# Kernel optimization log

Hardware: AMD Instinct MI355X
Metric: run time of the kernel (lower is better)

Reference implementation:

```python
import jax, jax.numpy as jnp
import numpy as np

N = 20000
MOL = 16
MH = 64      # message_hidden
UH = 64      # update_hidden
HEADS = 2
CUTOFF = 0.02257
E_FIX = 720000
REL_IN = 3 + 2 + MOL          # 21
SELF_F = 2 + MOL + 1 + 1      # 20
EDGE_A = MH + SELF_F          # 84
OUT_D = 2 + 1 + MOL + 1       # 20


def _build_edges(x_np, cutoff):
    """All ordered pairs (i,j), i!=j, with dist<=cutoff (matches symmetrized triu in torch)."""
    src_l, dst_l = [], []
    chunk = 1000
    Nn = x_np.shape[0]
    c2 = cutoff * cutoff
    for i0 in range(0, Nn, chunk):
        xi = x_np[i0:i0 + chunk]
        d2 = ((xi[:, None, :] - x_np[None, :, :]) ** 2).sum(-1)
        ii, jj = np.nonzero(d2 <= c2)
        ii = ii + i0
        keep = ii != jj
        dst_l.append(ii[keep])
        src_l.append(jj[keep])
    return (np.concatenate(src_l).astype(np.int32),
            np.concatenate(dst_l).astype(np.int32))


def setup_inputs() -> dict:
    key = jax.random.key(0)
    ks = jax.random.split(key, 30)
    x = jax.random.uniform(ks[0], (N, 2), dtype=jnp.float32)
    angle = jax.random.normal(ks[1], (N, 1), dtype=jnp.float32)
    molecules = jax.random.normal(ks[2], (N, MOL), dtype=jnp.float32)
    generation = jnp.zeros((N, 1), dtype=jnp.float32)

    src_np, dst_np = _build_edges(np.asarray(x), CUTOFF)
    E = min(src_np.shape[0], E_FIX)
    src = np.zeros(E_FIX, np.int32)
    dst = np.zeros(E_FIX, np.int32)
    mask = np.zeros(E_FIX, np.float32)
    src[:E] = src_np[:E]
    dst[:E] = dst_np[:E]
    mask[:E] = 1.0

    def p(k, shape):
        return jax.random.normal(k, shape, dtype=jnp.float32) * 0.05

    inp = dict(
        x=x, angle=angle, molecules=molecules, generation=generation,
        src=jnp.asarray(src), dst=jnp.asarray(dst), edge_mask=jnp.asarray(mask),
        # message_mlp
        mw1=p(ks[3], (REL_IN, MH)), mb1=p(ks[4], (MH,)),
        mw2=p(ks[5], (MH, MH)), mb2=p(ks[6], (MH,)),
        mw3=p(ks[7], (MH, MH)), mb3=p(ks[8], (MH,)),
        # TransformerConv (heads=2, out=UH, concat=False, edge_dim=EDGE_A)
        wq=p(ks[9], (SELF_F, HEADS * UH)), bq=p(ks[10], (HEADS * UH,)),
        wk=p(ks[11], (SELF_F, HEADS * UH)), bk=p(ks[12], (HEADS * UH,)),
        wv=p(ks[13], (SELF_F, HEADS * UH)), bv=p(ks[14], (HEADS * UH,)),
        we=p(ks[15], (EDGE_A, HEADS * UH)),  # lin_edge has no bias in PyG
        wskip=p(ks[16], (SELF_F, UH)), bskip=p(ks[17], (UH,)),
        # node_head
        hw1=p(ks[18], (UH, UH)), hb1=p(ks[19], (UH,)),
        hw2=p(ks[20], (UH, UH)), hb2=p(ks[21], (UH,)),
        hw3=p(ks[22], (UH, OUT_D)), hb3=p(ks[23], (OUT_D,)),
    )
    return inp


def reference(x, angle, molecules, generation, src, dst, edge_mask,
              mw1, mb1, mw2, mb2, mw3, mb3,
              wq, bq, wk, bk, wv, bv, we, wskip, bskip,
              hw1, hb1, hw2, hb2, hw3, hb3):
    Nn = x.shape[0]
    H, C = HEADS, UH
    m = edge_mask  # [E], 1 for real edges, 0 for padding

    # relative edge features (j = src = neighbor, i = dst = center)
    dxdy = x[src] - x[dst]                                          # [E,2]
    r = jnp.sqrt(jnp.clip((dxdy ** 2).sum(-1, keepdims=True), 1e-12))
    d_ang = angle[src] - angle[dst]                                 # [E,1]
    d_mol = molecules[src] - molecules[dst]                         # [E,MOL]
    rel_in = jnp.concatenate([dxdy, r, jnp.sin(d_ang), jnp.cos(d_ang), d_mol], -1)

    h = jax.nn.relu(rel_in @ mw1 + mb1)
    h = jax.nn.relu(h @ mw2 + mb2)
    msg = jax.nn.relu(h @ mw3 + mb3)                                # [E,MH]

    degree = jax.ops.segment_sum(m, dst, num_segments=Nn)[:, None]  # [N,1]
    self_feat = jnp.concatenate(
        [jnp.sin(angle), jnp.cos(angle), molecules, generation, degree], -1)  # [N,20]
    edge_attr = jnp.concatenate([msg, self_feat[dst]], -1)          # [E,84]

    # TransformerConv: q_i, (k_j + e), (v_j + e); per-dst segment softmax; mean heads; + skip
    q = (self_feat @ wq + bq).reshape(Nn, H, C)
    k = (self_feat @ wk + bk).reshape(Nn, H, C)
    v = (self_feat @ wv + bv).reshape(Nn, H, C)
    e = (edge_attr @ we).reshape(-1, H, C)
    key_e = k[src] + e
    val_e = v[src] + e
    alpha = (q[dst] * key_e).sum(-1) / jnp.sqrt(jnp.float32(C))     # [E,H]
    alpha = jnp.where(m[:, None] > 0, alpha, -1e9)
    amax = jax.ops.segment_max(alpha, dst, num_segments=Nn)         # [N,H]
    ex = jnp.exp(alpha - amax[dst]) * m[:, None]
    denom = jax.ops.segment_sum(ex, dst, num_segments=Nn)           # [N,H]
    w = ex / (denom[dst] + 1e-16)                                   # [E,H]
    out = jax.ops.segment_sum(val_e * w[:, :, None], dst, num_segments=Nn)  # [N,H,C]
    out = out.mean(axis=1) + (self_feat @ wskip + bskip)            # [N,UH]

    u = jax.nn.relu(out @ hw1 + hb1)
    u = jax.nn.relu(u @ hw2 + hb2)
    upd = u @ hw3 + hb3                                             # [N,20]

    return (upd[:, 0:2], upd[:, 2:3], upd[:, 3:3 + MOL], upd[:, 3 + MOL:4 + MOL])
```

## Files before the change

### kernel.cpp

```cpp
#include <hip/hip_runtime.h>
#include <hip/hip_bf16.h>
#include <math.h>

#define NN 20000
#define EF 720000

typedef float  f4 __attribute__((ext_vector_type(4)));
typedef unsigned int u4 __attribute__((ext_vector_type(4)));

__device__ __forceinline__ void MFMA(f4& c, u4 a, u4 b) {
    asm("v_mfma_f32_16x16x32_bf16 %0, %1, %2, %0" : "+v"(c) : "v"(a), "v"(b));
}

__device__ __forceinline__ unsigned pk(float a, float b) {
    __hip_bfloat162 t = __halves2bfloat162(__float2bfloat16(a), __float2bfloat16(b));
    unsigned u; __builtin_memcpy(&u, &t, 4); return u;
}
__device__ __forceinline__ float bf2f(unsigned short u) {
    return __builtin_bit_cast(float, (unsigned)u << 16);
}
__device__ __forceinline__ f4 bf2f4(ushort4 u) {
    f4 r; r.x = bf2f(u.x); r.y = bf2f(u.y); r.z = bf2f(u.z); r.w = bf2f(u.w); return r;
}
__device__ __forceinline__ float dot4(f4 a, f4 b) {
    return a.x * b.x + a.y * b.y + a.z * b.z + a.w * b.w;
}
__device__ __forceinline__ void fma4(f4& acc, float w, f4 v) {
    acc.x += w * v.x; acc.y += w * v.y; acc.z += w * v.z; acc.w += w * v.w;
}

__global__ __launch_bounds__(256) void k_prep(
    const float* __restrict__ mw1, const float* __restrict__ mb1,
    const float* __restrict__ mw2, const float* __restrict__ mw3,
    const float* __restrict__ hw1, const float* __restrict__ hw2, const float* __restrict__ hw3,
    const float* __restrict__ we, const float* __restrict__ wk, const float* __restrict__ bk,
    const float* __restrict__ wv, const float* __restrict__ bv,
    const float* __restrict__ wq, const float* __restrict__ bq,
    __hip_bfloat16* __restrict__ W1b, __hip_bfloat16* __restrict__ W2b, __hip_bfloat16* __restrict__ W3b,
    __hip_bfloat16* __restrict__ H1b, __hip_bfloat16* __restrict__ H2b, __hip_bfloat16* __restrict__ H3b,
    __hip_bfloat16* __restrict__ WcA, float* __restrict__ Mwe, float* __restrict__ Mk)
{
    int t = blockIdx.x * 256 + threadIdx.x;
    if (t < 2048) {
        int ch = t >> 5, k = t & 31;
        float v = (k < 21) ? mw1[k * 64 + ch] : (k == 21 ? mb1[ch] : 0.f);
        W1b[t] = __float2bfloat16(v); return;
    }
    t -= 2048;
    if (t < 4096) { int ch = t >> 6, k = t & 63; W2b[t] = __float2bfloat16(mw2[k * 64 + ch]); return; }
    t -= 4096;
    if (t < 4096) { int ch = t >> 6, k = t & 63; W3b[t] = __float2bfloat16(mw3[k * 64 + ch]); return; }
    t -= 4096;
    if (t < 4096) { int ch = t >> 6, k = t & 63; H1b[t] = __float2bfloat16(hw1[k * 64 + ch]); return; }
    t -= 4096;
    if (t < 4096) { int ch = t >> 6, k = t & 63; H2b[t] = __float2bfloat16(hw2[k * 64 + ch]); return; }
    t -= 4096;
    if (t < 2048) {
        int ch = t >> 6, k = t & 63;
        float v = (ch < 20) ? hw3[k * 20 + ch] : 0.f;
        H3b[t] = __float2bfloat16(v); return;
    }
    t -= 2048;
    if (t < 16384) {
        int h = t >> 13, rem = t & 8191;
        int ch = rem >> 7, k = rem & 127;
        int col = h * 64 + ch;
        float v;
        if (k < 64)        v = we[k * 128 + col];
        else if (k < 84)   v = wv[(k - 64) * 128 + col];
        else if (k == 84)  v = bv[col];
        else if (k < 96)   v = 0.f;
        else if (k < 116)  v = we[(64 + (k - 96)) * 128 + col];
        else               v = 0.f;
        WcA[t] = __float2bfloat16(v); return;
    }
    t -= 16384;
    if (t < 3528) {
        int j = t / 168, o = t % 168;
        int h = (o >= 84) ? 1 : 0, a = o - 84 * h;
        float acc = 0.f;
        for (int c = 0; c < 64; c++) {
            int hc = h * 64 + c;
            float wqv = (j < 20) ? wq[j * 128 + hc] : bq[hc];
            acc += wqv * we[a * 128 + hc];
        }
        Mwe[t] = acc; return;
    }
    t -= 3528;
    if (t < 1344) {
        int j = t / 64, rem = t % 64;
        int h = rem >> 5, a = rem & 31;
        float acc = 0.f;
        if (a <= 20) {
            for (int c = 0; c < 64; c++) {
                int hc = h * 64 + c;
                float wqv = (j < 20) ? wq[j * 128 + hc] : bq[hc];
                float wkv = (a < 20) ? wk[a * 128 + hc] : bk[hc];
                acc += wqv * wkv;
            }
        }
        Mk[t] = acc; return;
    }
}

__global__ __launch_bounds__(256) void k_csr(
    const int* __restrict__ dst, const float* __restrict__ mask, int* __restrict__ row_off)
{
    int n = blockIdx.x * 256 + threadIdx.x;
    if (n > NN) return;
    int lo = 0, hi = EF;
    while (lo < hi) { int mid = (lo + hi) >> 1; if (mask[mid] > 0.5f) lo = mid + 1; else hi = mid; }
    int Ea = lo;
    lo = 0; hi = Ea;
    while (lo < hi) { int mid = (lo + hi) >> 1; if (dst[mid] < n) lo = mid + 1; else hi = mid; }
    row_off[n] = lo;
}

__global__ __launch_bounds__(256) void k_node(
    const float* __restrict__ angle, const float* __restrict__ mol, const float* __restrict__ gen,
    const int* __restrict__ row_off,
    const float* __restrict__ wskip, const float* __restrict__ bskip,
    const float* __restrict__ Mwe, const float* __restrict__ Mk,
    float* __restrict__ selff, __hip_bfloat16* __restrict__ selffb,
    float* __restrict__ skipf, float* __restrict__ qwe, float* __restrict__ qkp)
{
    int wid = threadIdx.x >> 6, lane = threadIdx.x & 63;
    int n = blockIdx.x * 4 + wid;

    float an = angle[n];
    float sv, cv; sincosf(an, &sv, &cv);
    float degf = (float)(row_off[n + 1] - row_off[n]);
    float sfa[21];
    sfa[0] = sv; sfa[1] = cv;
#pragma unroll
    for (int j = 0; j < 16; j++) sfa[2 + j] = mol[n * 16 + j];
    sfa[18] = gen[n];
    sfa[19] = degf;
    sfa[20] = 1.f;

    float sval = (lane == 0) ? sv : (lane == 1) ? cv :
                 (lane < 18) ? mol[n * 16 + (lane - 2)] :
                 (lane == 18) ? gen[n] : degf;
    if (lane < 20) selff[n * 20 + lane] = sval;
    if (lane < 32) {
        float v = (lane < 20) ? sval : (lane == 20 ? 1.f : 0.f);
        selffb[n * 32 + lane] = __float2bfloat16(v);
    }

    float sk = bskip[lane];
#pragma unroll
    for (int j = 0; j < 20; j++) sk += sfa[j] * wskip[j * 64 + lane];
    skipf[n * 64 + lane] = sk;

#pragma unroll
    for (int r = 0; r < 3; r++) {
        int o = r * 64 + lane;
        if (o < 168) {
            float acc = 0.f;
#pragma unroll
            for (int j = 0; j < 21; j++) acc += sfa[j] * Mwe[j * 168 + o];
            qwe[n * 168 + o] = acc;
        }
    }

    {
        float acc = 0.f;
#pragma unroll
        for (int j = 0; j < 21; j++) acc += sfa[j] * Mk[j * 64 + lane];
        qkp[n * 64 + lane] = acc;
    }
}

__device__ __forceinline__ void write_tiles(char* lds, int l, f4 (&acc)[4][4], const float* bias)
{
#pragma unroll
    for (int m = 0; m < 4; m++) {
        f4 bv;
        if (bias) bv = *(const f4*)(bias + m * 16 + ((l >> 4) << 2));
        else      { bv.x = 0.f; bv.y = 0.f; bv.z = 0.f; bv.w = 0.f; }
#pragma unroll
        for (int n = 0; n < 4; n++) {
            f4 v = acc[m][n];
            float v0 = fmaxf(v.x + bv.x, 0.f);
            float v1 = fmaxf(v.y + bv.y, 0.f);
            float v2 = fmaxf(v.z + bv.z, 0.f);
            float v3 = fmaxf(v.w + bv.w, 0.f);
            int e   = n * 16 + (l & 15);
            int ch0 = m * 16 + ((l >> 4) << 2);
            int byte = e * 128 + ((((ch0 >> 3) ^ (e & 7))) << 4) + (ch0 & 7) * 2;
            uint2 w; w.x = pk(v0, v1); w.y = pk(v2, v3);
            *(uint2*)(lds + byte) = w;
        }
    }
}

__global__ __launch_bounds__(256) void k_edge_mfma(
    const float* __restrict__ x, const float* __restrict__ angle, const float* __restrict__ mol,
    const int* __restrict__ src, const int* __restrict__ dst,
    const float* __restrict__ mask,
    const __hip_bfloat16* __restrict__ W1b, const __hip_bfloat16* __restrict__ W2b,
    const __hip_bfloat16* __restrict__ W3b,
    const float* __restrict__ mb2, const float* __restrict__ mb3,
    __hip_bfloat16* __restrict__ msg)
{
    __shared__ char lds_all[4][64 * 128];
    int wv = threadIdx.x >> 6, l = threadIdx.x & 63;
    char* lds = lds_all[wv];
    int e0 = (blockIdx.x * 4 + wv) * 64;
    if (e0 + 64 > EF) e0 = EF - 64;

    if (mask[e0] < 0.5f) return;

    int s = src[e0 + l], d = dst[e0 + l];
    float2 xs = ((const float2*)x)[s], xd = ((const float2*)x)[d];
    float dx = xs.x - xd.x, dy = xs.y - xd.y;
    float r = sqrtf(fmaxf(dx * dx + dy * dy, 1e-12f));
    float da = angle[s] - angle[d];
    float sv, cv; sincosf(da, &sv, &cv);
    const float4* m4 = (const float4*)mol;
    float4 sa = m4[s * 4 + 0], sb = m4[s * 4 + 1], sc = m4[s * 4 + 2], sd = m4[s * 4 + 3];
    float4 ta = m4[d * 4 + 0], tb = m4[d * 4 + 1], tc = m4[d * 4 + 2], td = m4[d * 4 + 3];
    float f[22];
    f[0] = dx; f[1] = dy; f[2] = r; f[3] = sv; f[4] = cv;
    f[5]  = sa.x - ta.x; f[6]  = sa.y - ta.y; f[7]  = sa.z - ta.z; f[8]  = sa.w - ta.w;
    f[9]  = sb.x - tb.x; f[10] = sb.y - tb.y; f[11] = sb.z - tb.z; f[12] = sb.w - tb.w;
    f[13] = sc.x - tc.x; f[14] = sc.y - tc.y; f[15] = sc.z - tc.z; f[16] = sc.w - tc.w;
    f[17] = sd.x - td.x; f[18] = sd.y - td.y; f[19] = sd.z - td.z; f[20] = sd.w - td.w;
    f[21] = 1.f;
    unsigned p[16];
#pragma unroll
    for (int j = 0; j < 11; j++) p[j] = pk(f[2 * j], f[2 * j + 1]);
#pragma unroll
    for (int j = 11; j < 16; j++) p[j] = 0u;
#pragma unroll
    for (int g = 0; g < 4; g++) {
        int byte = l * 64 + ((g ^ (l & 3)) << 4);
        u4 w; w.x = p[4 * g]; w.y = p[4 * g + 1]; w.z = p[4 * g + 2]; w.w = p[4 * g + 3];
        *(u4*)(lds + byte) = w;
    }

    u4 B1[4];
#pragma unroll
    for (int n = 0; n < 4; n++) {
        int e = n * 16 + (l & 15);
        int byte = e * 64 + ((((l >> 4) & 3) ^ (e & 3)) << 4);
        B1[n] = *(const u4*)(lds + byte);
    }

    f4 acc[4][4];
#pragma unroll
    for (int m = 0; m < 4; m++)
#pragma unroll
        for (int n = 0; n < 4; n++) { acc[m][n].x = 0.f; acc[m][n].y = 0.f; acc[m][n].z = 0.f; acc[m][n].w = 0.f; }

    const unsigned short* W1u = (const unsigned short*)W1b;
    const unsigned short* W2u = (const unsigned short*)W2b;
    const unsigned short* W3u = (const unsigned short*)W3b;
#pragma unroll
    for (int m = 0; m < 4; m++) {
        u4 w = *(const u4*)(W1u + (m * 16 + (l & 15)) * 32 + (l >> 4) * 8);
#pragma unroll
        for (int n = 0; n < 4; n++) MFMA(acc[m][n], w, B1[n]);
    }
    write_tiles(lds, l, acc, nullptr);

    u4 B2[4][2];
#pragma unroll
    for (int n = 0; n < 4; n++)
#pragma unroll
        for (int ks = 0; ks < 2; ks++) {
            int e = n * 16 + (l & 15);
            int g = ks * 4 + (l >> 4);
            B2[n][ks] = *(const u4*)(lds + e * 128 + ((g ^ (e & 7)) << 4));
        }
#pragma unroll
    for (int m = 0; m < 4; m++)
#pragma unroll
        for (int n = 0; n < 4; n++) { acc[m][n].x = 0.f; acc[m][n].y = 0.f; acc[m][n].z = 0.f; acc[m][n].w = 0.f; }
#pragma unroll
    for (int m = 0; m < 4; m++)
#pragma unroll
        for (int ks = 0; ks < 2; ks++) {
            u4 w = *(const u4*)(W2u + (m * 16 + (l & 15)) * 64 + ks * 32 + (l >> 4) * 8);
#pragma unroll
            for (int n = 0; n < 4; n++) MFMA(acc[m][n], w, B2[n][ks]);
        }
    write_tiles(lds, l, acc, mb2);

#pragma unroll
    for (int n = 0; n < 4; n++)
#pragma unroll
        for (int ks = 0; ks < 2; ks++) {
            int e = n * 16 + (l & 15);
            int g = ks * 4 + (l >> 4);
            B2[n][ks] = *(const u4*)(lds + e * 128 + ((g ^ (e & 7)) << 4));
        }
#pragma unroll
    for (int m = 0; m < 4; m++)
#pragma unroll
        for (int n = 0; n < 4; n++) { acc[m][n].x = 0.f; acc[m][n].y = 0.f; acc[m][n].z = 0.f; acc[m][n].w = 0.f; }
#pragma unroll
    for (int m = 0; m < 4; m++)
#pragma unroll
        for (int ks = 0; ks < 2; ks++) {
            u4 w = *(const u4*)(W3u + (m * 16 + (l & 15)) * 64 + ks * 32 + (l >> 4) * 8);
#pragma unroll
            for (int n = 0; n < 4; n++) MFMA(acc[m][n], w, B2[n][ks]);
        }
    write_tiles(lds, l, acc, mb3);

#pragma unroll
    for (int it = 0; it < 8; it++) {
        int e = it * 8 + (l >> 3);
        int g = l & 7;
        u4 vv = *(const u4*)(lds + e * 128 + ((g ^ (e & 7)) << 4));
        *(u4*)((unsigned short*)msg + (size_t)(e0 + e) * 64 + g * 8) = vv;
    }
}

__global__ __launch_bounds__(256) void k_attn(
    const int* __restrict__ row_off, const int* __restrict__ src,
    const __hip_bfloat16* __restrict__ msg,
    const __hip_bfloat16* __restrict__ selffb, const float* __restrict__ qkp,
    const float* __restrict__ qwe, const float* __restrict__ selff,
    __hip_bfloat16* __restrict__ agg, float* __restrict__ invp)
{
    int tid = threadIdx.x, wid = tid >> 6, lane = tid & 63;
    int g = lane >> 4, c16 = lane & 15;
    int n = blockIdx.x * 4 + wid;

    f4 qm0 = *(const f4*)(qwe + n * 168 + 4 * c16);
    f4 qm1 = *(const f4*)(qwe + n * 168 + 84 + 4 * c16);
    float2 qk0 = *(const float2*)(qkp + n * 64 + 2 * c16);
    float2 qk1 = *(const float2*)(qkp + n * 64 + 32 + 2 * c16);

    float a00 = 0.f, a01 = 0.f;
#pragma unroll
    for (int j = 0; j < 20; j++) {
        float sfj = selff[n * 20 + j];
        a00 += sfj * qwe[n * 168 + 64 + j];
        a01 += sfj * qwe[n * 168 + 84 + 64 + j];
    }

    const unsigned short* msgu = (const unsigned short*)msg;
    const unsigned short* sfu  = (const unsigned short*)selffb;
    int r0 = row_off[n], r1 = row_off[n + 1];
    int nit = (r1 - r0 + 3) >> 2;

    f4 Wm0 = {0,0,0,0}, Wm1 = {0,0,0,0};
    float Ws00 = 0.f, Ws01 = 0.f, Ws10 = 0.f, Ws11 = 0.f;
    float S0 = 0.f, S1 = 0.f;

#pragma unroll 2
    for (int it = 0; it < nit; it++) {
        int e = r0 + it * 4 + g;
        bool ok = (e < r1);
        int ec = ok ? e : r0;
        int s = src[ec];
        ushort2 su = *(const ushort2*)(sfu + (size_t)s * 32 + 2 * c16);
        float sf0 = bf2f(su.x), sf1 = bf2f(su.y);
        f4 mc = bf2f4(*(const ushort4*)(msgu + (size_t)ec * 64 + 4 * c16));

        float t0 = dot4(qm0, mc) + sf0 * qk0.x + sf1 * qk0.y;
        float t1 = dot4(qm1, mc) + sf0 * qk1.x + sf1 * qk1.y;
#pragma unroll
        for (int mk = 1; mk < 16; mk <<= 1) {
            t0 += __shfl_xor(t0, mk, 64);
            t1 += __shfl_xor(t1, mk, 64);
        }
        float w0 = ok ? __expf((t0 + a00) * 0.125f) : 0.f;
        float w1 = ok ? __expf((t1 + a01) * 0.125f) : 0.f;
        S0 += w0; S1 += w1;
        fma4(Wm0, w0, mc); fma4(Wm1, w1, mc);
        Ws00 += w0 * sf0; Ws01 += w0 * sf1;
        Ws10 += w1 * sf0; Ws11 += w1 * sf1;
    }

#pragma unroll
    for (int mk = 16; mk <= 32; mk <<= 1) {
        Wm0.x += __shfl_xor(Wm0.x, mk, 64); Wm0.y += __shfl_xor(Wm0.y, mk, 64);
        Wm0.z += __shfl_xor(Wm0.z, mk, 64); Wm0.w += __shfl_xor(Wm0.w, mk, 64);
        Wm1.x += __shfl_xor(Wm1.x, mk, 64); Wm1.y += __shfl_xor(Wm1.y, mk, 64);
        Wm1.z += __shfl_xor(Wm1.z, mk, 64); Wm1.w += __shfl_xor(Wm1.w, mk, 64);
        Ws00 += __shfl_xor(Ws00, mk, 64); Ws01 += __shfl_xor(Ws01, mk, 64);
        Ws10 += __shfl_xor(Ws10, mk, 64); Ws11 += __shfl_xor(Ws11, mk, 64);
        S0 += __shfl_xor(S0, mk, 64); S1 += __shfl_xor(S1, mk, 64);
    }

    unsigned short* arow = (unsigned short*)agg + (size_t)n * 256;
    if (g == 0) {
        uint2 w; w.x = pk(Wm0.x, Wm0.y); w.y = pk(Wm0.z, Wm0.w);
        *(uint2*)(arow + 4 * c16) = w;
        int j0 = 2 * c16, j1 = 2 * c16 + 1;
        float v0 = (j0 < 20) ? S0 * selff[n * 20 + j0] : 0.f;
        float v1 = (j1 < 20) ? S0 * selff[n * 20 + j1] : 0.f;
        *(unsigned*)(arow + 96 + 2 * c16) = pk(v0, v1);
    } else if (g == 1) {
        uint2 w; w.x = pk(Wm1.x, Wm1.y); w.y = pk(Wm1.z, Wm1.w);
        *(uint2*)(arow + 128 + 4 * c16) = w;
        int j0 = 2 * c16, j1 = 2 * c16 + 1;
        float v0 = (j0 < 20) ? S1 * selff[n * 20 + j0] : 0.f;
        float v1 = (j1 < 20) ? S1 * selff[n * 20 + j1] : 0.f;
        *(unsigned*)(arow + 128 + 96 + 2 * c16) = pk(v0, v1);
    } else if (g == 2) {
        *(unsigned*)(arow + 64 + 2 * c16) = pk(Ws00, Ws01);
        if (c16 == 0) invp[2 * n] = 1.f / (S0 + 1e-16f);
    } else {
        *(unsigned*)(arow + 128 + 64 + 2 * c16) = pk(Ws10, Ws11);
        if (c16 == 0) invp[2 * n + 1] = 1.f / (S1 + 1e-16f);
    }
}

__global__ __launch_bounds__(64) void k_final2(
    const __hip_bfloat16* __restrict__ agg, const float* __restrict__ invp,
    const float* __restrict__ skipf, const __hip_bfloat16* __restrict__ WcA,
    const __hip_bfloat16* __restrict__ H1b, const __hip_bfloat16* __restrict__ H2b,
    const __hip_bfloat16* __restrict__ H3b,
    const float* __restrict__ hb1, const float* __restrict__ hb2, const float* __restrict__ hb3,
    float* __restrict__ out)
{
    __shared__ char lds[64 * 128];
    int l = threadIdx.x;
    int n0 = blockIdx.x * 64;

    const unsigned short* aggU = (const unsigned short*)agg;
    const unsigned short* WcU = (const unsigned short*)WcA;
    const unsigned short* H1u = (const unsigned short*)H1b;
    const unsigned short* H2u = (const unsigned short*)H2b;
    const unsigned short* H3u = (const unsigned short*)H3b;

    int nodes[4];
    float inv0[4], inv1[4];
#pragma unroll
    for (int n4 = 0; n4 < 4; n4++) {
        int node = n0 + n4 * 16 + (l & 15); if (node >= NN) node = NN - 1;
        nodes[n4] = node;
        float2 iv = *(const float2*)(invp + 2 * node);
        inv0[n4] = iv.x; inv1[n4] = iv.y;
    }

    f4 osum[4][4];
#pragma unroll
    for (int m = 0; m < 4; m++)
#pragma unroll
        for (int n4 = 0; n4 < 4; n4++) { osum[m][n4].x = 0.f; osum[m][n4].y = 0.f; osum[m][n4].z = 0.f; osum[m][n4].w = 0.f; }

#pragma unroll
    for (int h = 0; h < 2; h++) {
        f4 acc[4][4];
#pragma unroll
        for (int m = 0; m < 4; m++)
#pragma unroll
            for (int n4 = 0; n4 < 4; n4++) { acc[m][n4].x = 0.f; acc[m][n4].y = 0.f; acc[m][n4].z = 0.f; acc[m][n4].w = 0.f; }
#pragma unroll
        for (int ks = 0; ks < 4; ks++) {
            u4 A[4];
#pragma unroll
            for (int m = 0; m < 4; m++)
                A[m] = *(const u4*)(WcU + h * 8192 + (m * 16 + (l & 15)) * 128 + ks * 32 + (l >> 4) * 8);
#pragma unroll
            for (int n4 = 0; n4 < 4; n4++) {
                u4 B = *(const u4*)(aggU + (size_t)nodes[n4] * 256 + h * 128 + ks * 32 + (l >> 4) * 8);
#pragma unroll
                for (int m = 0; m < 4; m++) MFMA(acc[m][n4], A[m], B);
            }
        }
        const float* iv = h ? inv1 : inv0;
#pragma unroll
        for (int m = 0; m < 4; m++)
#pragma unroll
            for (int n4 = 0; n4 < 4; n4++) fma4(osum[m][n4], 0.5f * iv[n4], acc[m][n4]);
    }

#pragma unroll
    for (int m = 0; m < 4; m++) {
#pragma unroll
        for (int n4 = 0; n4 < 4; n4++) {
            int ch0 = m * 16 + ((l >> 4) << 2);
            float4 sk = *(const float4*)(skipf + (size_t)nodes[n4] * 64 + ch0);
            f4 v = osum[m][n4];
            float v0 = v.x + sk.x, v1 = v.y + sk.y, v2 = v.z + sk.z, v3 = v.w + sk.w;
            int e = n4 * 16 + (l & 15);
            int byte = e * 128 + ((((ch0 >> 3) ^ (e & 7))) << 4) + (ch0 & 7) * 2;
            uint2 w; w.x = pk(v0, v1); w.y = pk(v2, v3);
            *(uint2*)(lds + byte) = w;
        }
    }
    __syncthreads();

    u4 B[4][2];
    f4 acc[4][4];

#pragma unroll
    for (int n = 0; n < 4; n++)
#pragma unroll
        for (int ks = 0; ks < 2; ks++) {
            int e = n * 16 + (l & 15);
            int g = ks * 4 + (l >> 4);
            B[n][ks] = *(const u4*)(lds + e * 128 + ((g ^ (e & 7)) << 4));
        }
    __syncthreads();
#pragma unroll
    for (int m = 0; m < 4; m++)
#pragma unroll
        for (int n = 0; n < 4; n++) { acc[m][n].x = 0.f; acc[m][n].y = 0.f; acc[m][n].z = 0.f; acc[m][n].w = 0.f; }
#pragma unroll
    for (int m = 0; m < 4; m++)
#pragma unroll
        for (int ks = 0; ks < 2; ks++) {
            u4 w = *(const u4*)(H1u + (m * 16 + (l & 15)) * 64 + ks * 32 + (l >> 4) * 8);
#pragma unroll
            for (int n = 0; n < 4; n++) MFMA(acc[m][n], w, B[n][ks]);
        }
    write_tiles(lds, l, acc, hb1);
    __syncthreads();

#pragma unroll
    for (int n = 0; n < 4; n++)
#pragma unroll
        for (int ks = 0; ks < 2; ks++) {
            int e = n * 16 + (l & 15);
            int g = ks * 4 + (l >> 4);
            B[n][ks] = *(const u4*)(lds + e * 128 + ((g ^ (e & 7)) << 4));
        }
    __syncthreads();
#pragma unroll
    for (int m = 0; m < 4; m++)
#pragma unroll
        for (int n = 0; n < 4; n++) { acc[m][n].x = 0.f; acc[m][n].y = 0.f; acc[m][n].z = 0.f; acc[m][n].w = 0.f; }
#pragma unroll
    for (int m = 0; m < 4; m++)
#pragma unroll
        for (int ks = 0; ks < 2; ks++) {
            u4 w = *(const u4*)(H2u + (m * 16 + (l & 15)) * 64 + ks * 32 + (l >> 4) * 8);
#pragma unroll
            for (int n = 0; n < 4; n++) MFMA(acc[m][n], w, B[n][ks]);
        }
    write_tiles(lds, l, acc, hb2);
    __syncthreads();

#pragma unroll
    for (int n = 0; n < 4; n++)
#pragma unroll
        for (int ks = 0; ks < 2; ks++) {
            int e = n * 16 + (l & 15);
            int g = ks * 4 + (l >> 4);
            B[n][ks] = *(const u4*)(lds + e * 128 + ((g ^ (e & 7)) << 4));
        }

    f4 acc3[2][4];
#pragma unroll
    for (int m = 0; m < 2; m++)
#pragma unroll
        for (int n = 0; n < 4; n++) { acc3[m][n].x = 0.f; acc3[m][n].y = 0.f; acc3[m][n].z = 0.f; acc3[m][n].w = 0.f; }
#pragma unroll
    for (int m = 0; m < 2; m++)
#pragma unroll
        for (int ks = 0; ks < 2; ks++) {
            u4 w = *(const u4*)(H3u + (m * 16 + (l & 15)) * 64 + ks * 32 + (l >> 4) * 8);
#pragma unroll
            for (int n = 0; n < 4; n++) MFMA(acc3[m][n], w, B[n][ks]);
        }

#pragma unroll
    for (int m = 0; m < 2; m++) {
#pragma unroll
        for (int j = 0; j < 4; j++) {
            int ch = m * 16 + (l >> 4) * 4 + j;
            if (ch < 20) {
                float b = hb3[ch];
#pragma unroll
                for (int nt = 0; nt < 4; nt++) {
                    int node = n0 + nt * 16 + (l & 15);
                    if (node < NN) {
                        float v = acc3[m][nt][j] + b;
                        if (ch < 2)       out[node * 2 + ch] = v;
                        else if (ch == 2) out[2 * NN + node] = v;
                        else if (ch < 19) out[3 * NN + node * 16 + (ch - 3)] = v;
                        else              out[19 * NN + node] = v;
                    }
                }
            }
        }
    }
}

extern "C" void kernel_launch(void* const* d_in, const int* in_sizes, int n_in,
                              void* d_out, int out_size, void* d_ws, size_t ws_size,
                              hipStream_t stream)
{
    const float* x      = (const float*)d_in[0];
    const float* angle  = (const float*)d_in[1];
    const float* mol    = (const float*)d_in[2];
    const float* gen    = (const float*)d_in[3];
    const int*   src    = (const int*)d_in[4];
    const int*   dst    = (const int*)d_in[5];
    const float* mask   = (const float*)d_in[6];
    const float* mw1    = (const float*)d_in[7];
    const float* mb1    = (const float*)d_in[8];
    const float* mw2    = (const float*)d_in[9];
    const float* mb2    = (const float*)d_in[10];
    const float* mw3    = (const float*)d_in[11];
    const float* mb3    = (const float*)d_in[12];
    const float* wq     = (const float*)d_in[13];
    const float* bq     = (const float*)d_in[14];
    const float* wk     = (const float*)d_in[15];
    const float* bk     = (const float*)d_in[16];
    const float* wv     = (const float*)d_in[17];
    const float* bv     = (const float*)d_in[18];
    const float* we     = (const float*)d_in[19];
    const float* wskip  = (const float*)d_in[20];
    const float* bskip  = (const float*)d_in[21];
    const float* hw1    = (const float*)d_in[22];
    const float* hb1    = (const float*)d_in[23];
    const float* hw2    = (const float*)d_in[24];
    const float* hb2    = (const float*)d_in[25];
    const float* hw3    = (const float*)d_in[26];
    const float* hb3    = (const float*)d_in[27];
    float* out = (float*)d_out;

    char* p = (char*)d_ws;
    auto alloc = [&](size_t bytes) -> void* {
        void* r = (void*)p;
        p += (bytes + 255) & ~(size_t)255;
        return r;
    };
    int*   row_off = (int*)alloc((NN + 1) * 4);
    float* selff   = (float*)alloc((size_t)NN * 20 * 4);
    __hip_bfloat16* selffb = (__hip_bfloat16*)alloc((size_t)NN * 32 * 2);
    float* qkp     = (float*)alloc((size_t)NN * 64 * 4);
    float* skipf   = (float*)alloc((size_t)NN * 64 * 4);
    float* qwe     = (float*)alloc((size_t)NN * 168 * 4);
    __hip_bfloat16* agg = (__hip_bfloat16*)alloc((size_t)NN * 256 * 2);
    float* invp    = (float*)alloc((size_t)NN * 2 * 4);
    __hip_bfloat16* W1b = (__hip_bfloat16*)alloc(2048 * 2);
    __hip_bfloat16* W2b = (__hip_bfloat16*)alloc(4096 * 2);
    __hip_bfloat16* W3b = (__hip_bfloat16*)alloc(4096 * 2);
    __hip_bfloat16* H1b = (__hip_bfloat16*)alloc(4096 * 2);
    __hip_bfloat16* H2b = (__hip_bfloat16*)alloc(4096 * 2);
    __hip_bfloat16* H3b = (__hip_bfloat16*)alloc(2048 * 2);
    __hip_bfloat16* WcA = (__hip_bfloat16*)alloc(16384 * 2);
    float* Mwe     = (float*)alloc(3528 * 4);
    float* Mk      = (float*)alloc(1344 * 4);
    __hip_bfloat16* msg = (__hip_bfloat16*)alloc((size_t)EF * 64 * 2);

    k_prep<<<164, 256, 0, stream>>>(mw1, mb1, mw2, mw3, hw1, hw2, hw3, we, wk, bk, wv, bv,
                                    wq, bq, W1b, W2b, W3b, H1b, H2b, H3b, WcA, Mwe, Mk);
    k_csr<<<(NN + 256) / 256, 256, 0, stream>>>(dst, mask, row_off);
    k_node<<<NN / 4, 256, 0, stream>>>(angle, mol, gen, row_off,
                                       wskip, bskip, Mwe, Mk,
                                       selff, selffb, skipf, qwe, qkp);
    k_edge_mfma<<<(EF / 64 + 3) / 4, 256, 0, stream>>>(x, angle, mol, src, dst, mask,
                                                       W1b, W2b, W3b, mb2, mb3, msg);
    k_attn<<<NN / 4, 256, 0, stream>>>(row_off, src, msg, selffb, qkp,
                                       qwe, selff, agg, invp);
    k_final2<<<(NN + 63) / 64, 64, 0, stream>>>(agg, invp, skipf, WcA,
                                                H1b, H2b, H3b, hb1, hb2, hb3, out);
}
```

Measured before the change: 146.0 us.

## Process eight edges per wavefront iteration in attention with 8-lane groups

The attention kernel now assigns 8 lanes per edge, so each lane holds 8 message channels, instead of 16 lanes with 4 channels each. A wavefront therefore handles 8 edges per loop iteration, and each lane issues one 16-byte message load. The qwe row stride is padded from 168 to 192 so the per-head query vectors stay 16-byte aligned, which means the prep and node kernels change to match. The intent is fewer loop iterations and shorter reduction chains per edge, in exchange for more registers per lane and more cross-lane shuffles in the final reduction.

```diff
diff --git a/kernel.cpp b/kernel.cpp
--- a/kernel.cpp
+++ b/kernel.cpp
@@ -19,14 +19,9 @@
 __device__ __forceinline__ float bf2f(unsigned short u) {
     return __builtin_bit_cast(float, (unsigned)u << 16);
 }
-__device__ __forceinline__ f4 bf2f4(ushort4 u) {
-    f4 r; r.x = bf2f(u.x); r.y = bf2f(u.y); r.z = bf2f(u.z); r.w = bf2f(u.w); return r;
-}
-__device__ __forceinline__ float dot4(f4 a, f4 b) {
-    return a.x * b.x + a.y * b.y + a.z * b.z + a.w * b.w;
-}
-__device__ __forceinline__ void fma4(f4& acc, float w, f4 v) {
-    acc.x += w * v.x; acc.y += w * v.y; acc.z += w * v.z; acc.w += w * v.w;
+__device__ __forceinline__ unsigned short f2bfu(float f) {
+    __hip_bfloat16 b = __float2bfloat16(f);
+    unsigned short u; __builtin_memcpy(&u, &b, 2); return u;
 }
 
 __global__ __launch_bounds__(256) void k_prep(
@@ -75,18 +70,20 @@
         WcA[t] = __float2bfloat16(v); return;
     }
     t -= 16384;
-    if (t < 3528) {
-        int j = t / 168, o = t % 168;
-        int h = (o >= 84) ? 1 : 0, a = o - 84 * h;
+    if (t < 4032) {
+        int j = t / 192, o = t % 192;
+        int h = (o >= 96) ? 1 : 0, a = o - 96 * h;
         float acc = 0.f;
-        for (int c = 0; c < 64; c++) {
-            int hc = h * 64 + c;
-            float wqv = (j < 20) ? wq[j * 128 + hc] : bq[hc];
-            acc += wqv * we[a * 128 + hc];
+        if (a < 84) {
+            for (int c = 0; c < 64; c++) {
+                int hc = h * 64 + c;
+                float wqv = (j < 20) ? wq[j * 128 + hc] : bq[hc];
+                acc += wqv * we[a * 128 + hc];
+            }
         }
         Mwe[t] = acc; return;
     }
-    t -= 3528;
+    t -= 4032;
     if (t < 1344) {
         int j = t / 64, rem = t % 64;
         int h = rem >> 5, a = rem & 31;
@@ -155,12 +152,10 @@
 #pragma unroll
     for (int r = 0; r < 3; r++) {
         int o = r * 64 + lane;
-        if (o < 168) {
-            float acc = 0.f;
-#pragma unroll
-            for (int j = 0; j < 21; j++) acc += sfa[j] * Mwe[j * 168 + o];
-            qwe[n * 168 + o] = acc;
-        }
+        float acc = 0.f;
+#pragma unroll
+        for (int j = 0; j < 21; j++) acc += sfa[j] * Mwe[j * 192 + o];
+        qwe[n * 192 + o] = acc;
     }
 
     {
@@ -326,88 +321,118 @@
     __hip_bfloat16* __restrict__ agg, float* __restrict__ invp)
 {
     int tid = threadIdx.x, wid = tid >> 6, lane = tid & 63;
-    int g = lane >> 4, c16 = lane & 15;
+    int g = lane >> 3, c8 = lane & 7;
     int n = blockIdx.x * 4 + wid;
 
-    f4 qm0 = *(const f4*)(qwe + n * 168 + 4 * c16);
-    f4 qm1 = *(const f4*)(qwe + n * 168 + 84 + 4 * c16);
-    float2 qk0 = *(const float2*)(qkp + n * 64 + 2 * c16);
-    float2 qk1 = *(const float2*)(qkp + n * 64 + 32 + 2 * c16);
+    const float* qrow = qwe + (size_t)n * 192;
+    f4 qmA0 = *(const f4*)(qrow + 8 * c8);
+    f4 qmA1 = *(const f4*)(qrow + 8 * c8 + 4);
+    f4 qmB0 = *(const f4*)(qrow + 96 + 8 * c8);
+    f4 qmB1 = *(const f4*)(qrow + 96 + 8 * c8 + 4);
+    float qk0a = qkp[n * 64 + c8],      qk0b = qkp[n * 64 + c8 + 8],      qk0c = qkp[n * 64 + c8 + 16];
+    float qk1a = qkp[n * 64 + 32 + c8], qk1b = qkp[n * 64 + 32 + c8 + 8], qk1c = qkp[n * 64 + 32 + c8 + 16];
 
     float a00 = 0.f, a01 = 0.f;
 #pragma unroll
     for (int j = 0; j < 20; j++) {
         float sfj = selff[n * 20 + j];
-        a00 += sfj * qwe[n * 168 + 64 + j];
-        a01 += sfj * qwe[n * 168 + 84 + 64 + j];
+        a00 += sfj * qrow[64 + j];
+        a01 += sfj * qrow[96 + 64 + j];
     }
 
     const unsigned short* msgu = (const unsigned short*)msg;
     const unsigned short* sfu  = (const unsigned short*)selffb;
     int r0 = row_off[n], r1 = row_off[n + 1];
-    int nit = (r1 - r0 + 3) >> 2;
-
-    f4 Wm0 = {0,0,0,0}, Wm1 = {0,0,0,0};
-    float Ws00 = 0.f, Ws01 = 0.f, Ws10 = 0.f, Ws11 = 0.f;
+    int nit = (r1 - r0 + 7) >> 3;
+
+    f4 WmA0 = {0,0,0,0}, WmA1 = {0,0,0,0}, WmB0 = {0,0,0,0}, WmB1 = {0,0,0,0};
+    float Ws0a = 0.f, Ws0b = 0.f, Ws0c = 0.f, Ws1a = 0.f, Ws1b = 0.f, Ws1c = 0.f;
     float S0 = 0.f, S1 = 0.f;
 
 #pragma unroll 2
     for (int it = 0; it < nit; it++) {
-        int e = r0 + it * 4 + g;
+        int e = r0 + it * 8 + g;
         bool ok = (e < r1);
         int ec = ok ? e : r0;
         int s = src[ec];
-        ushort2 su = *(const ushort2*)(sfu + (size_t)s * 32 + 2 * c16);
-        float sf0 = bf2f(su.x), sf1 = bf2f(su.y);
-        f4 mc = bf2f4(*(const ushort4*)(msgu + (size_t)ec * 64 + 4 * c16));
-
-        float t0 = dot4(qm0, mc) + sf0 * qk0.x + sf1 * qk0.y;
-        float t1 = dot4(qm1, mc) + sf0 * qk1.x + sf1 * qk1.y;
-#pragma unroll
-        for (int mk = 1; mk < 16; mk <<= 1) {
+        float sfA = bf2f(sfu[(size_t)s * 32 + c8]);
+        float sfB = bf2f(sfu[(size_t)s * 32 + c8 + 8]);
+        float sfC = bf2f(sfu[(size_t)s * 32 + c8 + 16]);
+        u4 mr = *(const u4*)(msgu + (size_t)ec * 64 + 8 * c8);
+        float c0 = __builtin_bit_cast(float, mr.x << 16);
+        float c1 = __builtin_bit_cast(float, mr.x & 0xffff0000u);
+        float c2 = __builtin_bit_cast(float, mr.y << 16);
+        float c3 = __builtin_bit_cast(float, mr.y & 0xffff0000u);
+        float c4 = __builtin_bit_cast(float, mr.z << 16);
+        float c5 = __builtin_bit_cast(float, mr.z & 0xffff0000u);
+        float c6 = __builtin_bit_cast(float, mr.w << 16);
+        float c7 = __builtin_bit_cast(float, mr.w & 0xffff0000u);
+
+        float t0 = qmA0.x * c0 + qmA0.y * c1 + qmA0.z * c2 + qmA0.w * c3
+                 + qmA1.x * c4 + qmA1.y * c5 + qmA1.z * c6 + qmA1.w * c7
+                 + sfA * qk0a + sfB * qk0b + sfC * qk0c;
+        float t1 = qmB0.x * c0 + qmB0.y * c1 + qmB0.z * c2 + qmB0.w * c3
+                 + qmB1.x * c4 + qmB1.y * c5 + qmB1.z * c6 + qmB1.w * c7
+                 + sfA * qk1a + sfB * qk1b + sfC * qk1c;
+#pragma unroll
+        for (int mk = 1; mk < 8; mk <<= 1) {
             t0 += __shfl_xor(t0, mk, 64);
             t1 += __shfl_xor(t1, mk, 64);
         }
         float w0 = ok ? __expf((t0 + a00) * 0.125f) : 0.f;
         float w1 = ok ? __expf((t1 + a01) * 0.125f) : 0.f;
         S0 += w0; S1 += w1;
-        fma4(Wm0, w0, mc); fma4(Wm1, w1, mc);
-        Ws00 += w0 * sf0; Ws01 += w0 * sf1;
-        Ws10 += w1 * sf0; Ws11 += w1 * sf1;
-    }
-
-#pragma unroll
-    for (int mk = 16; mk <= 32; mk <<= 1) {
-        Wm0.x += __shfl_xor(Wm0.x, mk, 64); Wm0.y += __shfl_xor(Wm0.y, mk, 64);
-        Wm0.z += __shfl_xor(Wm0.z, mk, 64); Wm0.w += __shfl_xor(Wm0.w, mk, 64);
-        Wm1.x += __shfl_xor(Wm1.x, mk, 64); Wm1.y += __shfl_xor(Wm1.y, mk, 64);
-        Wm1.z += __shfl_xor(Wm1.z, mk, 64); Wm1.w += __shfl_xor(Wm1.w, mk, 64);
-        Ws00 += __shfl_xor(Ws00, mk, 64); Ws01 += __shfl_xor(Ws01, mk, 64);
-        Ws10 += __shfl_xor(Ws10, mk, 64); Ws11 += __shfl_xor(Ws11, mk, 64);
+        WmA0.x += w0 * c0; WmA0.y += w0 * c1; WmA0.z += w0 * c2; WmA0.w += w0 * c3;
+        WmA1.x += w0 * c4; WmA1.y += w0 * c5; WmA1.z += w0 * c6; WmA1.w += w0 * c7;
+        WmB0.x += w1 * c0; WmB0.y += w1 * c1; WmB0.z += w1 * c2; WmB0.w += w1 * c3;
+        WmB1.x += w1 * c4; WmB1.y += w1 * c5; WmB1.z += w1 * c6; WmB1.w += w1 * c7;
+        Ws0a += w0 * sfA; Ws0b += w0 * sfB; Ws0c += w0 * sfC;
+        Ws1a += w1 * sfA; Ws1b += w1 * sfB; Ws1c += w1 * sfC;
+    }
+
+#pragma unroll
+    for (int mk = 8; mk <= 32; mk <<= 1) {
+        WmA0.x += __shfl_xor(WmA0.x, mk, 64); WmA0.y += __shfl_xor(WmA0.y, mk, 64);
+        WmA0.z += __shfl_xor(WmA0.z, mk, 64); WmA0.w += __shfl_xor(WmA0.w, mk, 64);
+        WmA1.x += __shfl_xor(WmA1.x, mk, 64); WmA1.y += __shfl_xor(WmA1.y, mk, 64);
+        WmA1.z += __shfl_xor(WmA1.z, mk, 64); WmA1.w += __shfl_xor(WmA1.w, mk, 64);
+        WmB0.x += __shfl_xor(WmB0.x, mk, 64); WmB0.y += __shfl_xor(WmB0.y, mk, 64);
+        WmB0.z += __shfl_xor(WmB0.z, mk, 64); WmB0.w += __shfl_xor(WmB0.w, mk, 64);
+        WmB1.x += __shfl_xor(WmB1.x, mk, 64); WmB1.y += __shfl_xor(WmB1.y, mk, 64);
+        WmB1.z += __shfl_xor(WmB1.z, mk, 64); WmB1.w += __shfl_xor(WmB1.w, mk, 64);
+        Ws0a += __shfl_xor(Ws0a, mk, 64); Ws0b += __shfl_xor(Ws0b, mk, 64); Ws0c += __shfl_xor(Ws0c, mk, 64);
+        Ws1a += __shfl_xor(Ws1a, mk, 64); Ws1b += __shfl_xor(Ws1b, mk, 64); Ws1c += __shfl_xor(Ws1c, mk, 64);
         S0 += __shfl_xor(S0, mk, 64); S1 += __shfl_xor(S1, mk, 64);
     }
 
     unsigned short* arow = (unsigned short*)agg + (size_t)n * 256;
     if (g == 0) {
-        uint2 w; w.x = pk(Wm0.x, Wm0.y); w.y = pk(Wm0.z, Wm0.w);
-        *(uint2*)(arow + 4 * c16) = w;
-        int j0 = 2 * c16, j1 = 2 * c16 + 1;
-        float v0 = (j0 < 20) ? S0 * selff[n * 20 + j0] : 0.f;
-        float v1 = (j1 < 20) ? S0 * selff[n * 20 + j1] : 0.f;
-        *(unsigned*)(arow + 96 + 2 * c16) = pk(v0, v1);
+        u4 w; w.x = pk(WmA0.x, WmA0.y); w.y = pk(WmA0.z, WmA0.w);
+        w.z = pk(WmA1.x, WmA1.y); w.w = pk(WmA1.z, WmA1.w);
+        *(u4*)(arow + 8 * c8) = w;
     } else if (g == 1) {
-        uint2 w; w.x = pk(Wm1.x, Wm1.y); w.y = pk(Wm1.z, Wm1.w);
-        *(uint2*)(arow + 128 + 4 * c16) = w;
-        int j0 = 2 * c16, j1 = 2 * c16 + 1;
-        float v0 = (j0 < 20) ? S1 * selff[n * 20 + j0] : 0.f;
-        float v1 = (j1 < 20) ? S1 * selff[n * 20 + j1] : 0.f;
-        *(unsigned*)(arow + 128 + 96 + 2 * c16) = pk(v0, v1);
+        u4 w; w.x = pk(WmB0.x, WmB0.y); w.y = pk(WmB0.z, WmB0.w);
+        w.z = pk(WmB1.x, WmB1.y); w.w = pk(WmB1.z, WmB1.w);
+        *(u4*)(arow + 128 + 8 * c8) = w;
     } else if (g == 2) {
-        *(unsigned*)(arow + 64 + 2 * c16) = pk(Ws00, Ws01);
-        if (c16 == 0) invp[2 * n] = 1.f / (S0 + 1e-16f);
-    } else {
-        *(unsigned*)(arow + 128 + 64 + 2 * c16) = pk(Ws10, Ws11);
-        if (c16 == 0) invp[2 * n + 1] = 1.f / (S1 + 1e-16f);
+        arow[64 + c8]      = f2bfu(Ws0a);
+        arow[64 + c8 + 8]  = f2bfu(Ws0b);
+        arow[64 + c8 + 16] = f2bfu(Ws0c);
+    } else if (g == 3) {
+        arow[128 + 64 + c8]      = f2bfu(Ws1a);
+        arow[128 + 64 + c8 + 8]  = f2bfu(Ws1b);
+        arow[128 + 64 + c8 + 16] = f2bfu(Ws1c);
+    } else if (g == 4) {
+        arow[96 + c8]     = f2bfu(S0 * selff[n * 20 + c8]);
+        arow[96 + c8 + 8] = f2bfu(S0 * selff[n * 20 + c8 + 8]);
+        if (c8 < 4) arow[96 + c8 + 16] = f2bfu(S0 * selff[n * 20 + c8 + 16]);
+    } else if (g == 5) {
+        arow[128 + 96 + c8]     = f2bfu(S1 * selff[n * 20 + c8]);
+        arow[128 + 96 + c8 + 8] = f2bfu(S1 * selff[n * 20 + c8 + 8]);
+        if (c8 < 4) arow[128 + 96 + c8 + 16] = f2bfu(S1 * selff[n * 20 + c8 + 16]);
+    } else if (g == 6 && c8 == 0) {
+        invp[2 * n]     = 1.f / (S0 + 1e-16f);
+        invp[2 * n + 1] = 1.f / (S1 + 1e-16f);
     }
 }
 
@@ -469,7 +494,11 @@
 #pragma unroll
         for (int m = 0; m < 4; m++)
 #pragma unroll
-            for (int n4 = 0; n4 < 4; n4++) fma4(osum[m][n4], 0.5f * iv[n4], acc[m][n4]);
+            for (int n4 = 0; n4 < 4; n4++) {
+                float s = 0.5f * iv[n4];
+                osum[m][n4].x += s * acc[m][n4].x; osum[m][n4].y += s * acc[m][n4].y;
+                osum[m][n4].z += s * acc[m][n4].z; osum[m][n4].w += s * acc[m][n4].w;
+            }
     }
 
 #pragma unroll
@@ -630,7 +659,7 @@
     __hip_bfloat16* selffb = (__hip_bfloat16*)alloc((size_t)NN * 32 * 2);
     float* qkp     = (float*)alloc((size_t)NN * 64 * 4);
     float* skipf   = (float*)alloc((size_t)NN * 64 * 4);
-    float* qwe     = (float*)alloc((size_t)NN * 168 * 4);
+    float* qwe     = (float*)alloc((size_t)NN * 192 * 4);
     __hip_bfloat16* agg = (__hip_bfloat16*)alloc((size_t)NN * 256 * 2);
     float* invp    = (float*)alloc((size_t)NN * 2 * 4);
     __hip_bfloat16* W1b = (__hip_bfloat16*)alloc(2048 * 2);
@@ -640,11 +669,11 @@
     __hip_bfloat16* H2b = (__hip_bfloat16*)alloc(4096 * 2);
     __hip_bfloat16* H3b = (__hip_bfloat16*)alloc(2048 * 2);
     __hip_bfloat16* WcA = (__hip_bfloat16*)alloc(16384 * 2);
-    float* Mwe     = (float*)alloc(3528 * 4);
+    float* Mwe     = (float*)alloc(4032 * 4);
     float* Mk      = (float*)alloc(1344 * 4);
     __hip_bfloat16* msg = (__hip_bfloat16*)alloc((size_t)EF * 64 * 2);
 
-    k_prep<<<164, 256, 0, stream>>>(mw1, mb1, mw2, mw3, hw1, hw2, hw3, we, wk, bk, wv, bv,
+    k_prep<<<165, 256, 0, stream>>>(mw1, mb1, mw2, mw3, hw1, hw2, hw3, we, wk, bk, wv, bv,
                                     wq, bq, W1b, W2b, W3b, H1b, H2b, H3b, WcA, Mwe, Mk);
     k_csr<<<(NN + 256) / 256, 256, 0, stream>>>(dst, mask, row_off);
     k_node<<<NN / 4, 256, 0, stream>>>(angle, mol, gen, row_off,
```

Measured after the change: 146.4 us. Within noise of the previous version (+0.3%).
